# Performance work log

Hardware: AMD Instinct MI355X
Metric: run time of the kernel (lower is better)

## Reference

```python
import jax, jax.numpy as jnp
import numpy as np

D_MODEL = 512
PROJ = 2 * D_MODEL  # 1024
N_STATES = 32
KSIZE = 4
LN_EPS = 1e-3  # keras LayerNormalization default epsilon


def setup_inputs() -> dict:
    key = jax.random.key(0)
    ks = jax.random.split(key, 16)
    B, L = 2, 2048
    s_in = 1.0 / np.sqrt(D_MODEL)
    s_pr = 1.0 / np.sqrt(PROJ)
    x = jax.random.normal(ks[0], (B, L, D_MODEL), dtype=jnp.float32)
    # LayerNorm params
    ln_gamma = jnp.ones((D_MODEL,), jnp.float32)
    ln_beta = jnp.zeros((D_MODEL,), jnp.float32)
    # dense1 / dense2: d_model -> proj
    W1 = jax.random.normal(ks[1], (D_MODEL, PROJ), jnp.float32) * s_in
    b1 = jnp.zeros((PROJ,), jnp.float32)
    W2 = jax.random.normal(ks[2], (D_MODEL, PROJ), jnp.float32) * s_in
    b2 = jnp.zeros((PROJ,), jnp.float32)
    # depthwise causal conv1d: kernel (K, 1, PROJ) in WIO layout, groups=PROJ
    conv_k = jax.random.normal(ks[3], (KSIZE, 1, PROJ), jnp.float32) * 0.5
    conv_b = jnp.zeros((PROJ,), jnp.float32)
    # SSM params
    A_log = jnp.log(jnp.broadcast_to(jnp.arange(1, N_STATES + 1, dtype=jnp.float32), (PROJ, N_STATES)))
    D_skip = jnp.ones((PROJ,), jnp.float32)
    WB = jax.random.normal(ks[4], (PROJ, N_STATES), jnp.float32) * s_pr
    bB = jnp.zeros((N_STATES,), jnp.float32)
    WC = jax.random.normal(ks[5], (PROJ, N_STATES), jnp.float32) * s_pr
    bC = jnp.zeros((N_STATES,), jnp.float32)
    Wd = jax.random.normal(ks[6], (PROJ, PROJ), jnp.float32) * s_pr
    bd = jnp.zeros((PROJ,), jnp.float32)
    # dense3: proj -> d_model
    W3 = jax.random.normal(ks[7], (PROJ, D_MODEL), jnp.float32) * s_pr
    b3 = jnp.zeros((D_MODEL,), jnp.float32)
    return dict(x=x, ln_gamma=ln_gamma, ln_beta=ln_beta, W1=W1, b1=b1, W2=W2, b2=b2,
                conv_k=conv_k, conv_b=conv_b, A_log=A_log, D_skip=D_skip,
                WB=WB, bB=bB, WC=WC, bC=bC, Wd=Wd, bd=bd, W3=W3, b3=b3)


def _layernorm(x, gamma, beta):
    mu = jnp.mean(x, axis=-1, keepdims=True)
    var = jnp.mean(jnp.square(x - mu), axis=-1, keepdims=True)
    return (x - mu) * jax.lax.rsqrt(var + LN_EPS) * gamma + beta


def _causal_dwconv(x, k, b):
    # x: [B,L,C], k: [K,1,C], depthwise causal conv (left-pad K-1)
    y = jax.lax.conv_general_dilated(
        x, k, window_strides=(1,), padding=[(KSIZE - 1, 0)],
        dimension_numbers=('NWC', 'WIO', 'NWC'), feature_group_count=PROJ)
    return y + b


def _selective_scan(u, delta, A, Bm, Cm, D_skip):
    # u, delta: [B,L,D]; A: [D,N]; Bm, Cm: [B,L,N]; D_skip: [D]
    deltaA = jnp.einsum('bld,dn->bldn', delta, A)                 # [B,L,D,N]
    deltaBu = jnp.einsum('bld,bld,bln->bldn', delta, u, Bm)        # [B,L,D,N]
    # shift deltaA left by one along L, zero at the end (pad trick in source)
    shifted = jnp.concatenate([deltaA[:, 1:], jnp.zeros_like(deltaA[:, :1])], axis=1)
    # reversed cumsum along L, then exp
    e = jnp.exp(jnp.flip(jnp.cumsum(jnp.flip(shifted, axis=1), axis=1), axis=1))
    xs = jnp.cumsum(deltaBu * e, axis=1) / (e + 1e-12)
    y = jnp.einsum('bldn,bln->bld', xs, Cm)
    return y + u * D_skip


def reference(x, ln_gamma, ln_beta, W1, b1, W2, b2, conv_k, conv_b,
              A_log, D_skip, WB, bB, WC, bC, Wd, bd, W3, b3):
    h = _layernorm(x, ln_gamma, ln_beta)
    x1 = h @ W1 + b1                      # [B,L,PROJ]
    x1 = _causal_dwconv(x1, conv_k, conv_b)
    x1 = jax.nn.silu(x1)
    A = -jnp.exp(A_log)                    # [PROJ,N]
    Cm = x1 @ WC + bC                      # [B,L,N]
    Bm = x1 @ WB + bB                      # [B,L,N]
    delta = jax.nn.softplus(x1 @ Wd + bd)  # [B,L,PROJ]
    y = _selective_scan(x1, delta, A, Bm, Cm, D_skip)
    x2 = jax.nn.silu(h @ W2 + b2)
    out = (y * x2) @ W3 + b3 + x           # residual; dropout is identity at inference
    return out
```

## Files before the change

### kernel.cpp

```cpp
#include <hip/hip_runtime.h>
#include <stdint.h>

#define L_SEQ 2048
#define BATCH 2
#define DMODEL 512
#define PROJ 1024
#define NST 32
#define NCAT 1152
#define ROWS (BATCH*L_SEQ)
#define THRESH 50.0f

typedef float f32x4 __attribute__((ext_vector_type(4)));
typedef short short8 __attribute__((ext_vector_type(8)));

__device__ inline float bf2f(unsigned short u){ uint32_t x=((uint32_t)u)<<16; float f; __builtin_memcpy(&f,&x,4); return f; }
__device__ inline unsigned short f2bf(float f){ uint32_t x; __builtin_memcpy(&x,&f,4); uint32_t r=x+0x7FFFu+((x>>16)&1u); return (unsigned short)(r>>16); }
__device__ inline float siluf(float x){ return x/(1.f+__expf(-x)); }
__device__ inline float softplusf(float x){ return x>20.f? x : log1pf(__expf(x)); }

#define AS1(p) ((const __attribute__((address_space(1))) void*)(p))
#define AS3(p) ((__attribute__((address_space(3))) void*)(p))

template<int N> __device__ inline void wait_vmcnt(){
  if constexpr (N==0)      asm volatile("s_waitcnt vmcnt(0)" ::: "memory");
  else if constexpr (N==1) asm volatile("s_waitcnt vmcnt(1)" ::: "memory");
  else if constexpr (N==2) asm volatile("s_waitcnt vmcnt(2)" ::: "memory");
  else if constexpr (N==3) asm volatile("s_waitcnt vmcnt(3)" ::: "memory");
  else if constexpr (N==4) asm volatile("s_waitcnt vmcnt(4)" ::: "memory");
  else if constexpr (N==5) asm volatile("s_waitcnt vmcnt(5)" ::: "memory");
  else if constexpr (N==6) asm volatile("s_waitcnt vmcnt(6)" ::: "memory");
  else                     asm volatile("s_waitcnt vmcnt(8)" ::: "memory");
}

__global__ __launch_bounds__(256)
void prep_kernel(const float* __restrict__ W1, const float* __restrict__ b1,
                 const float* __restrict__ W2, const float* __restrict__ b2,
                 const float* __restrict__ Wd, const float* __restrict__ bd,
                 const float* __restrict__ WB, const float* __restrict__ bB,
                 const float* __restrict__ WC, const float* __restrict__ bC,
                 const float* __restrict__ W3,
                 unsigned short* __restrict__ W12t, unsigned short* __restrict__ Wcatt,
                 unsigned short* __restrict__ W3t, float* __restrict__ bias12,
                 float* __restrict__ biascat)
{
  int i = blockIdx.x*256 + threadIdx.x;
  const int nA = 2048*512;
  const int nB = NCAT*1024;
  const int nC = 512*1024;
  if (i < nA) {
    int n = i >> 9, k = i & 511;
    float v = (n < 1024) ? W1[k*1024 + n] : W2[k*1024 + (n-1024)];
    W12t[i] = f2bf(v);
    return;
  }
  i -= nA;
  if (i < nB) {
    int n = i >> 10, k = i & 1023;
    float v;
    if (n < 1024) v = Wd[k*1024 + n];
    else if (n < 1056) v = WB[k*32 + (n-1024)];
    else if (n < 1088) v = WC[k*32 + (n-1056)];
    else v = 0.f;
    Wcatt[i] = f2bf(v);
    return;
  }
  i -= nB;
  if (i < nC) {
    int n = i >> 10, k = i & 1023;
    W3t[i] = f2bf(W3[k*512 + n]);
    return;
  }
  i -= nC;
  if (i < 2048) { bias12[i] = (i < 1024) ? b1[i] : b2[i-1024]; return; }
  i -= 2048;
  if (i < NCAT) {
    biascat[i] = (i < 1024) ? bd[i] : (i < 1056) ? bB[i-1024] : (i < 1088) ? bC[i-1056] : 0.f;
  }
}

__global__ __launch_bounds__(256)
void ln_kernel(const float* __restrict__ x, const float* __restrict__ gamma,
               const float* __restrict__ beta, unsigned short* __restrict__ H)
{
  int row = blockIdx.x*4 + (threadIdx.x >> 6);
  int lane = threadIdx.x & 63;
  const float4* xr = (const float4*)(x + (size_t)row*DMODEL);
  float4 v0 = xr[lane];
  float4 v1 = xr[lane+64];
  float s = v0.x+v0.y+v0.z+v0.w + v1.x+v1.y+v1.z+v1.w;
  float q = v0.x*v0.x+v0.y*v0.y+v0.z*v0.z+v0.w*v0.w
          + v1.x*v1.x+v1.y*v1.y+v1.z*v1.z+v1.w*v1.w;
#pragma unroll
  for (int m=32;m>0;m>>=1){ s += __shfl_xor(s,m); q += __shfl_xor(q,m); }
  float mu = s*(1.f/DMODEL);
  float var = q*(1.f/DMODEL) - mu*mu;
  float rs = rsqrtf(var + 1e-3f);
  int c0 = lane*4, c1 = 256 + lane*4;
  float4 g0 = *(const float4*)&gamma[c0]; float4 g1 = *(const float4*)&gamma[c1];
  float4 t0 = *(const float4*)&beta[c0];  float4 t1 = *(const float4*)&beta[c1];
  ushort4 o0, o1;
  o0.x = f2bf((v0.x-mu)*rs*g0.x + t0.x);
  o0.y = f2bf((v0.y-mu)*rs*g0.y + t0.y);
  o0.z = f2bf((v0.z-mu)*rs*g0.z + t0.z);
  o0.w = f2bf((v0.w-mu)*rs*g0.w + t0.w);
  o1.x = f2bf((v1.x-mu)*rs*g1.x + t1.x);
  o1.y = f2bf((v1.y-mu)*rs*g1.y + t1.y);
  o1.z = f2bf((v1.z-mu)*rs*g1.z + t1.z);
  o1.w = f2bf((v1.w-mu)*rs*g1.w + t1.w);
  *(ushort4*)&H[(size_t)row*DMODEL + c0] = o0;
  *(ushort4*)&H[(size_t)row*DMODEL + c1] = o1;
}

template<int BM, int BN, int WR, int WC, int MODE>
__global__ __launch_bounds__(256)
void gemm_bt(const unsigned short* __restrict__ A, const unsigned short* __restrict__ Bt,
             void* __restrict__ Cv, const float* __restrict__ bias,
             const float* __restrict__ res, int M, int N, int K)
{
  constexpr int BMW = BM/WR, BNW = BN/WC;
  constexpr int AM = BMW/16, AN = BNW/16;
  constexpr int ASEGI = BM*4/256;
  constexpr int BSEGI = BN*4/256;
  constexpr int LPT = ASEGI + BSEGI;
  __shared__ unsigned short As[3][BM*32];
  __shared__ unsigned short Bs[3][BN*32];
  int tid = threadIdx.x;
  int lane = tid & 63, wid = tid >> 6;
  int wm = wid / WC, wn = wid % WC;
  int m0 = blockIdx.x*BM, n0 = blockIdx.y*BN;

  f32x4 acc[AM][AN];
#pragma unroll
  for (int i=0;i<AM;i++)
#pragma unroll
    for (int j=0;j<AN;j++)
#pragma unroll
      for (int e=0;e<4;e++) acc[i][j][e] = 0.f;

  const unsigned short* ap[ASEGI];
  const unsigned short* bp[BSEGI];
#pragma unroll
  for (int j=0;j<ASEGI;j++){
    int s = tid + j*256;
    int row = s >> 2, kc = ((s & 3) ^ (row & 3)) * 8;
    ap[j] = A + (size_t)(m0+row)*K + kc;
  }
#pragma unroll
  for (int j=0;j<BSEGI;j++){
    int s = tid + j*256;
    int row = s >> 2, kc = ((s & 3) ^ (row & 3)) * 8;
    bp[j] = Bt + (size_t)(n0+row)*K + kc;
  }

  auto stage = [&](int buf){
#pragma unroll
    for (int j=0;j<ASEGI;j++){
      __builtin_amdgcn_global_load_lds(AS1(ap[j]), AS3(&As[buf][(size_t)(wid*64 + j*256)*8]), 16, 0, 0);
      ap[j] += 32;
    }
#pragma unroll
    for (int j=0;j<BSEGI;j++){
      __builtin_amdgcn_global_load_lds(AS1(bp[j]), AS3(&Bs[buf][(size_t)(wid*64 + j*256)*8]), 16, 0, 0);
      bp[j] += 32;
    }
  };

  stage(0);
  stage(1);
  int T = K/32;
  int rb = 0, wb = 2;
  int r = lane & 15, kb = lane >> 4;
  int kbx = kb ^ (r & 3);
  for (int t = 0; t < T; ++t) {
    if (t+1 < T) wait_vmcnt<LPT>();
    else         wait_vmcnt<0>();
    __builtin_amdgcn_s_barrier();
    if (t+2 < T) { stage(wb); wb = (wb==2)?0:wb+1; }
    short8 af[AM], bfr[AN];
#pragma unroll
    for (int i=0;i<AM;i++) af[i]  = *(const short8*)&As[rb][((wm*BMW + i*16 + r)*4 + kbx)*8];
#pragma unroll
    for (int j=0;j<AN;j++) bfr[j] = *(const short8*)&Bs[rb][((wn*BNW + j*16 + r)*4 + kbx)*8];
#pragma unroll
    for (int i=0;i<AM;i++)
#pragma unroll
      for (int j=0;j<AN;j++)
        acc[i][j] = __builtin_amdgcn_mfma_f32_16x16x32_bf16(af[i], bfr[j], acc[i][j], 0,0,0);
    rb = (rb==2)?0:rb+1;
  }

  int rr = (lane >> 4)*4, cc = lane & 15;
#pragma unroll
  for (int i=0;i<AM;i++)
#pragma unroll
    for (int j=0;j<AN;j++) {
      int col = n0 + wn*BNW + j*16 + cc;
      float bv = bias[col];
#pragma unroll
      for (int e=0;e<4;e++) {
        int row = m0 + wm*BMW + i*16 + rr + e;
        float v = acc[i][j][e] + bv;
        if (MODE == 0) {
          ((unsigned short*)Cv)[(size_t)row*N + col] = f2bf(v);
        } else if (MODE == 2) {
          if (col < 1024) v = softplusf(v);
          ((float*)Cv)[(size_t)row*N + col] = v;
        } else {
          v += res[(size_t)row*N + col];
          ((float*)Cv)[(size_t)row*N + col] = v;
        }
      }
    }
}

__global__ __launch_bounds__(256)
void conv_silu_kernel(const unsigned short* __restrict__ P12, const float* __restrict__ ck,
                      const float* __restrict__ cb, unsigned short* __restrict__ ubf,
                      unsigned short* __restrict__ x2bf)
{
  int gid = blockIdx.x*256 + threadIdx.x;
  int c4 = gid & 511;
  int row = gid >> 9;
  int l = row & (L_SEQ-1);
  if (c4 < 256) {
    int c = c4*4;
    float4 bv = *(const float4*)&cb[c];
    float r0=bv.x, r1=bv.y, r2=bv.z, r3=bv.w;
#pragma unroll
    for (int t=0;t<4;t++){
      int lsrc = l - 3 + t;
      if (lsrc >= 0) {
        ushort4 xv = *(const ushort4*)&P12[(size_t)(row-3+t)*2048 + c];
        float4 kv = *(const float4*)&ck[t*PROJ + c];
        r0 = fmaf(bf2f(xv.x),kv.x,r0);
        r1 = fmaf(bf2f(xv.y),kv.y,r1);
        r2 = fmaf(bf2f(xv.z),kv.z,r2);
        r3 = fmaf(bf2f(xv.w),kv.w,r3);
      }
    }
    ushort4 o;
    o.x=f2bf(siluf(r0)); o.y=f2bf(siluf(r1)); o.z=f2bf(siluf(r2)); o.w=f2bf(siluf(r3));
    *(ushort4*)&ubf[(size_t)row*PROJ + c] = o;
  } else {
    int c = (c4-256)*4;
    ushort4 xv = *(const ushort4*)&P12[(size_t)row*2048 + 1024 + c];
    ushort4 o;
    o.x=f2bf(siluf(bf2f(xv.x))); o.y=f2bf(siluf(bf2f(xv.y)));
    o.z=f2bf(siluf(bf2f(xv.z))); o.w=f2bf(siluf(bf2f(xv.w)));
    *(ushort4*)&x2bf[(size_t)row*PROJ + c] = o;
  }
}

__global__ __launch_bounds__(256)
void dtrans_kernel(const float* __restrict__ P3, float* __restrict__ deltaT)
{
  __shared__ float tile[32][33];
  int bz = blockIdx.z;
  int l0t = blockIdx.x*32, d0t = blockIdx.y*32;
  int lx = threadIdx.x & 31, ly = threadIdx.x >> 5;
#pragma unroll
  for (int i=0;i<4;i++)
    tile[ly+i*8][lx] = P3[(size_t)(bz*L_SEQ + l0t + ly + i*8)*NCAT + d0t + lx];
  __syncthreads();
#pragma unroll
  for (int i=0;i<4;i++)
    deltaT[(size_t)(bz*PROJ + d0t + ly + i*8)*L_SEQ + l0t + lx] = tile[lx][ly+i*8];
}

__global__ __launch_bounds__(256)
void tsum_kernel(const float* __restrict__ deltaT, float* __restrict__ sufshT,
                 int* __restrict__ l0out)
{
  int G = blockIdx.x;
  const float* row = deltaT + (size_t)G*L_SEQ;
  int t = threadIdx.x;
  float4 v0 = *(const float4*)&row[t*8];
  float4 v1 = *(const float4*)&row[t*8+4];
  float vals[8] = {v0.x,v0.y,v0.z,v0.w,v1.x,v1.y,v1.z,v1.w};
  float part = 0.f;
#pragma unroll
  for (int i=0;i<8;i++) part += vals[i];
  __shared__ float ps[256];
  ps[t] = part; __syncthreads();
  for (int off=1; off<256; off<<=1){
    float v = (t >= off) ? ps[t-off] : 0.f;
    __syncthreads();
    ps[t] += v;
    __syncthreads();
  }
  float T = ps[255];
  float prefx = ps[t] - part;
  float run = prefx; int cnt = 0; float out[8];
#pragma unroll
  for (int i=0;i<8;i++){
    float suf_l = T - run;
    cnt += (suf_l >= THRESH) ? 1 : 0;
    run += vals[i];
    out[i] = T - run;
  }
  *(float4*)&sufshT[(size_t)G*L_SEQ + t*8]     = make_float4(out[0],out[1],out[2],out[3]);
  *(float4*)&sufshT[(size_t)G*L_SEQ + t*8 + 4] = make_float4(out[4],out[5],out[6],out[7]);
  __shared__ int cs[256];
  cs[t] = cnt; __syncthreads();
  for (int off=128; off>0; off>>=1){ if (t < off) cs[t] += cs[t+off]; __syncthreads(); }
  if (t == 0) {
    int total = cs[0];
    l0out[G] = total > 0 ? total-1 : 0;
  }
}

__global__ __launch_bounds__(256)
void scan_kernel(const float* __restrict__ deltaT, const float* __restrict__ sufshT,
                 const float* __restrict__ P3, const unsigned short* __restrict__ ubf,
                 const float* __restrict__ A_log, const int* __restrict__ l0arr,
                 float* __restrict__ ystate)
{
  int tid = threadIdx.x;
  int n = tid & 31;
  int G = blockIdx.x*8 + (tid >> 5);
  int b = G >> 10, d = G & 1023;
  float np1 = __expf(A_log[d*NST + n]);
  int myl0 = l0arr[G];
  int base = min(myl0, __shfl_xor(myl0, 32)) & ~7;
  const float* dT = deltaT + (size_t)G*L_SEQ;
  const float* sT = sufshT + (size_t)G*L_SEQ;
  const float* P3b = P3 + (size_t)b*L_SEQ*NCAT + 1024 + n;
  const unsigned short* ub = ubf + (size_t)b*L_SEQ*PROJ + d;
  float* yb = ystate + (size_t)b*L_SEQ*PROJ + d;
  float s = 0.f;
  for (int l = base; l < L_SEQ; l += 8) {
    float4 d0 = *(const float4*)&dT[l];
    float4 d1 = *(const float4*)&dT[l+4];
    float4 f0 = *(const float4*)&sT[l];
    float4 f1 = *(const float4*)&sT[l+4];
    float dl[8] = {d0.x,d0.y,d0.z,d0.w,d1.x,d1.y,d1.z,d1.w};
    float sf[8] = {f0.x,f0.y,f0.z,f0.w,f1.x,f1.y,f1.z,f1.w};
    float uu[8], Bv[8], Cv[8];
#pragma unroll
    for (int t=0;t<8;t++){
      uu[t] = bf2f(ub[(size_t)(l+t)*PROJ]);
      const float* rp = P3b + (size_t)(l+t)*NCAT;
      Bv[t] = rp[0];
      Cv[t] = rp[32];
    }
#pragma unroll
    for (int t=0;t<8;t++){
      float decay = __expf(-dl[t]*np1);
      s = fmaf(decay, s, dl[t]*uu[t]*Bv[t]);
      float gte = 1.f/(1.f + 1e-12f*__expf(np1*sf[t]));
      float contrib = s*gte*Cv[t];
#pragma unroll
      for (int m=16;m>0;m>>=1) contrib += __shfl_xor(contrib, m);
      if (n == 0) yb[(size_t)(l+t)*PROJ] = contrib;
    }
  }
}

__global__ __launch_bounds__(256)
void zmul_kernel(const float* __restrict__ ystate, const unsigned short* __restrict__ ubf,
                 const unsigned short* __restrict__ x2bf, const float* __restrict__ Dskip,
                 unsigned short* __restrict__ zbf)
{
  size_t i = ((size_t)blockIdx.x*256 + threadIdx.x)*4;
  int d = (int)(i & (PROJ-1));
  float4 ys = *(const float4*)&ystate[i];
  ushort4 uu = *(const ushort4*)&ubf[i];
  ushort4 xx = *(const ushort4*)&x2bf[i];
  float4 Dv = *(const float4*)&Dskip[d];
  ushort4 o;
  o.x = f2bf((ys.x + bf2f(uu.x)*Dv.x)*bf2f(xx.x));
  o.y = f2bf((ys.y + bf2f(uu.y)*Dv.y)*bf2f(xx.y));
  o.z = f2bf((ys.z + bf2f(uu.z)*Dv.z)*bf2f(xx.z));
  o.w = f2bf((ys.w + bf2f(uu.w)*Dv.w)*bf2f(xx.w));
  *(ushort4*)&zbf[i] = o;
}

extern "C" void kernel_launch(void* const* d_in, const int* in_sizes, int n_in,
                              void* d_out, int out_size, void* d_ws, size_t ws_size,
                              hipStream_t stream)
{
  const float* x     = (const float*)d_in[0];
  const float* ln_g  = (const float*)d_in[1];
  const float* ln_b  = (const float*)d_in[2];
  const float* W1    = (const float*)d_in[3];
  const float* b1    = (const float*)d_in[4];
  const float* W2    = (const float*)d_in[5];
  const float* b2    = (const float*)d_in[6];
  const float* convk = (const float*)d_in[7];
  const float* convb = (const float*)d_in[8];
  const float* A_log = (const float*)d_in[9];
  const float* Dskip = (const float*)d_in[10];
  const float* WB    = (const float*)d_in[11];
  const float* bB    = (const float*)d_in[12];
  const float* WC    = (const float*)d_in[13];
  const float* bC    = (const float*)d_in[14];
  const float* Wd    = (const float*)d_in[15];
  const float* bd    = (const float*)d_in[16];
  const float* W3    = (const float*)d_in[17];
  const float* b3    = (const float*)d_in[18];

  char* w = (char*)d_ws;
  auto alloc = [&](size_t bytes){ char* p = w; w += (bytes + 255) & ~(size_t)255; return p; };
  unsigned short* Hbf    = (unsigned short*)alloc((size_t)ROWS*DMODEL*2);
  unsigned short* W12t   = (unsigned short*)alloc((size_t)2048*512*2);
  unsigned short* Wcatt  = (unsigned short*)alloc((size_t)NCAT*1024*2);
  unsigned short* W3t    = (unsigned short*)alloc((size_t)512*1024*2);
  float*          bias12 = (float*)alloc(2048*4);
  float*          biascat= (float*)alloc(NCAT*4);
  unsigned short* P12    = (unsigned short*)alloc((size_t)ROWS*2048*2);
  unsigned short* ubf    = (unsigned short*)alloc((size_t)ROWS*PROJ*2);
  unsigned short* x2bf   = (unsigned short*)alloc((size_t)ROWS*PROJ*2);
  float*          P3     = (float*)alloc((size_t)ROWS*NCAT*4);
  float*          deltaT = (float*)alloc((size_t)2048*L_SEQ*4);
  float*          sufshT = (float*)alloc((size_t)2048*L_SEQ*4);
  int*            l0arr  = (int*)alloc(2048*4);
  float*          ystate = (float*)alloc((size_t)ROWS*PROJ*4);
  unsigned short* zbf    = (unsigned short*)alloc((size_t)ROWS*PROJ*2);

  {
    int total = 2048*512 + NCAT*1024 + 512*1024 + 2048 + NCAT;
    prep_kernel<<<(total+255)/256, 256, 0, stream>>>(W1,b1,W2,b2,Wd,bd,WB,bB,WC,bC,W3,
                                                     W12t,Wcatt,W3t,bias12,biascat);
  }
  ln_kernel<<<ROWS/4, 256, 0, stream>>>(x, ln_g, ln_b, Hbf);

  dim3 g1(ROWS/64, 2048/128);
  gemm_bt<64,128,2,2,0><<<g1, 256, 0, stream>>>(Hbf, W12t, P12, bias12, nullptr, ROWS, 2048, DMODEL);

  conv_silu_kernel<<<ROWS*512/256, 256, 0, stream>>>(P12, convk, convb, ubf, x2bf);

  dim3 g2(ROWS/64, NCAT/64);
  gemm_bt<64,64,2,2,2><<<g2, 256, 0, stream>>>(ubf, Wcatt, P3, biascat, nullptr, ROWS, NCAT, PROJ);

  hipMemsetAsync(ystate, 0, (size_t)ROWS*PROJ*4, stream);

  dim3 gt(L_SEQ/32, PROJ/32, BATCH);
  dtrans_kernel<<<gt, 256, 0, stream>>>(P3, deltaT);

  tsum_kernel<<<2048, 256, 0, stream>>>(deltaT, sufshT, l0arr);

  scan_kernel<<<2048/8, 256, 0, stream>>>(deltaT, sufshT, P3, ubf, A_log, l0arr, ystate);

  zmul_kernel<<<(ROWS*PROJ/4)/256, 256, 0, stream>>>(ystate, ubf, x2bf, Dskip, zbf);

  dim3 g3(ROWS/64, DMODEL/64);
  gemm_bt<64,64,2,2,3><<<g3, 256, 0, stream>>>(zbf, W3t, (float*)d_out, b3, x, ROWS, DMODEL, PROJ);
}
```

Baseline: 163.6 us.

## Retile GEMMs to 2-wave row-split blocks and drop ystate memset via l0 masking

The GEMM kernel is restructured so each block uses a configurable number of waves, each owning a stripe of rows across the full block width. The first two GEMMs move to 128x64 tiles with 128 threads, and the last to 64x64 with 128 threads. Separately, the memset that zeroed the scan output buffer is removed; the elementwise z kernel now masks ystate entries before each channel's l0 start index, avoiding a full-buffer write. Smaller blocks change occupancy and per-wave register use, and correctness now depends on the scan not leaving stale data beyond the masked region.

```diff
diff --git a/kernel.cpp b/kernel.cpp
--- a/kernel.cpp
+++ b/kernel.cpp
@@ -111,22 +111,22 @@
   *(ushort4*)&H[(size_t)row*DMODEL + c1] = o1;
 }
 
-template<int BM, int BN, int WR, int WC, int MODE>
-__global__ __launch_bounds__(256)
+template<int BM, int BN, int WAVES, int MODE>
+__global__ __launch_bounds__(WAVES*64)
 void gemm_bt(const unsigned short* __restrict__ A, const unsigned short* __restrict__ Bt,
              void* __restrict__ Cv, const float* __restrict__ bias,
              const float* __restrict__ res, int M, int N, int K)
 {
-  constexpr int BMW = BM/WR, BNW = BN/WC;
-  constexpr int AM = BMW/16, AN = BNW/16;
-  constexpr int ASEGI = BM*4/256;
-  constexpr int BSEGI = BN*4/256;
+  constexpr int THREADS = WAVES*64;
+  constexpr int BMW = BM/WAVES;
+  constexpr int AM = BMW/16, AN = BN/16;
+  constexpr int ASEGI = BM*4/THREADS;
+  constexpr int BSEGI = BN*4/THREADS;
   constexpr int LPT = ASEGI + BSEGI;
   __shared__ unsigned short As[3][BM*32];
   __shared__ unsigned short Bs[3][BN*32];
   int tid = threadIdx.x;
   int lane = tid & 63, wid = tid >> 6;
-  int wm = wid / WC, wn = wid % WC;
   int m0 = blockIdx.x*BM, n0 = blockIdx.y*BN;
 
   f32x4 acc[AM][AN];
@@ -141,13 +141,13 @@
   const unsigned short* bp[BSEGI];
 #pragma unroll
   for (int j=0;j<ASEGI;j++){
-    int s = tid + j*256;
+    int s = tid + j*THREADS;
     int row = s >> 2, kc = ((s & 3) ^ (row & 3)) * 8;
     ap[j] = A + (size_t)(m0+row)*K + kc;
   }
 #pragma unroll
   for (int j=0;j<BSEGI;j++){
-    int s = tid + j*256;
+    int s = tid + j*THREADS;
     int row = s >> 2, kc = ((s & 3) ^ (row & 3)) * 8;
     bp[j] = Bt + (size_t)(n0+row)*K + kc;
   }
@@ -155,12 +155,12 @@
   auto stage = [&](int buf){
 #pragma unroll
     for (int j=0;j<ASEGI;j++){
-      __builtin_amdgcn_global_load_lds(AS1(ap[j]), AS3(&As[buf][(size_t)(wid*64 + j*256)*8]), 16, 0, 0);
+      __builtin_amdgcn_global_load_lds(AS1(ap[j]), AS3(&As[buf][(size_t)(j*THREADS + wid*64)*8]), 16, 0, 0);
       ap[j] += 32;
     }
 #pragma unroll
     for (int j=0;j<BSEGI;j++){
-      __builtin_amdgcn_global_load_lds(AS1(bp[j]), AS3(&Bs[buf][(size_t)(wid*64 + j*256)*8]), 16, 0, 0);
+      __builtin_amdgcn_global_load_lds(AS1(bp[j]), AS3(&Bs[buf][(size_t)(j*THREADS + wid*64)*8]), 16, 0, 0);
       bp[j] += 32;
     }
   };
@@ -178,9 +178,9 @@
     if (t+2 < T) { stage(wb); wb = (wb==2)?0:wb+1; }
     short8 af[AM], bfr[AN];
 #pragma unroll
-    for (int i=0;i<AM;i++) af[i]  = *(const short8*)&As[rb][((wm*BMW + i*16 + r)*4 + kbx)*8];
-#pragma unroll
-    for (int j=0;j<AN;j++) bfr[j] = *(const short8*)&Bs[rb][((wn*BNW + j*16 + r)*4 + kbx)*8];
+    for (int i=0;i<AM;i++) af[i]  = *(const short8*)&As[rb][((wid*BMW + i*16 + r)*4 + kbx)*8];
+#pragma unroll
+    for (int j=0;j<AN;j++) bfr[j] = *(const short8*)&Bs[rb][((j*16 + r)*4 + kbx)*8];
 #pragma unroll
     for (int i=0;i<AM;i++)
 #pragma unroll
@@ -194,11 +194,11 @@
   for (int i=0;i<AM;i++)
 #pragma unroll
     for (int j=0;j<AN;j++) {
-      int col = n0 + wn*BNW + j*16 + cc;
+      int col = n0 + j*16 + cc;
       float bv = bias[col];
 #pragma unroll
       for (int e=0;e<4;e++) {
-        int row = m0 + wm*BMW + i*16 + rr + e;
+        int row = m0 + wid*BMW + i*16 + rr + e;
         float v = acc[i][j][e] + bv;
         if (MODE == 0) {
           ((unsigned short*)Cv)[(size_t)row*N + col] = f2bf(v);
@@ -359,11 +359,19 @@
 __global__ __launch_bounds__(256)
 void zmul_kernel(const float* __restrict__ ystate, const unsigned short* __restrict__ ubf,
                  const unsigned short* __restrict__ x2bf, const float* __restrict__ Dskip,
-                 unsigned short* __restrict__ zbf)
+                 const int* __restrict__ l0arr, unsigned short* __restrict__ zbf)
 {
   size_t i = ((size_t)blockIdx.x*256 + threadIdx.x)*4;
   int d = (int)(i & (PROJ-1));
+  int row = (int)(i >> 10);
+  int l = row & (L_SEQ-1);
+  int b = row >> 11;
+  int4 l0v = *(const int4*)&l0arr[b*PROJ + d];
   float4 ys = *(const float4*)&ystate[i];
+  ys.x = (l >= l0v.x) ? ys.x : 0.f;
+  ys.y = (l >= l0v.y) ? ys.y : 0.f;
+  ys.z = (l >= l0v.z) ? ys.z : 0.f;
+  ys.w = (l >= l0v.w) ? ys.w : 0.f;
   ushort4 uu = *(const ushort4*)&ubf[i];
   ushort4 xx = *(const ushort4*)&x2bf[i];
   float4 Dv = *(const float4*)&Dskip[d];
@@ -424,15 +432,13 @@
   }
   ln_kernel<<<ROWS/4, 256, 0, stream>>>(x, ln_g, ln_b, Hbf);
 
-  dim3 g1(ROWS/64, 2048/128);
-  gemm_bt<64,128,2,2,0><<<g1, 256, 0, stream>>>(Hbf, W12t, P12, bias12, nullptr, ROWS, 2048, DMODEL);
+  dim3 g1(ROWS/128, 2048/64);
+  gemm_bt<128,64,2,0><<<g1, 128, 0, stream>>>(Hbf, W12t, P12, bias12, nullptr, ROWS, 2048, DMODEL);
 
   conv_silu_kernel<<<ROWS*512/256, 256, 0, stream>>>(P12, convk, convb, ubf, x2bf);
 
-  dim3 g2(ROWS/64, NCAT/64);
-  gemm_bt<64,64,2,2,2><<<g2, 256, 0, stream>>>(ubf, Wcatt, P3, biascat, nullptr, ROWS, NCAT, PROJ);
-
-  hipMemsetAsync(ystate, 0, (size_t)ROWS*PROJ*4, stream);
+  dim3 g2(ROWS/128, NCAT/64);
+  gemm_bt<128,64,2,2><<<g2, 128, 0, stream>>>(ubf, Wcatt, P3, biascat, nullptr, ROWS, NCAT, PROJ);
 
   dim3 gt(L_SEQ/32, PROJ/32, BATCH);
   dtrans_kernel<<<gt, 256, 0, stream>>>(P3, deltaT);
@@ -441,8 +447,8 @@
 
   scan_kernel<<<2048/8, 256, 0, stream>>>(deltaT, sufshT, P3, ubf, A_log, l0arr, ystate);
 
-  zmul_kernel<<<(ROWS*PROJ/4)/256, 256, 0, stream>>>(ystate, ubf, x2bf, Dskip, zbf);
+  zmul_kernel<<<(ROWS*PROJ/4)/256, 256, 0, stream>>>(ystate, ubf, x2bf, Dskip, l0arr, zbf);
 
   dim3 g3(ROWS/64, DMODEL/64);
-  gemm_bt<64,64,2,2,3><<<g3, 256, 0, stream>>>(zbf, W3t, (float*)d_out, b3, x, ROWS, DMODEL, PROJ);
-}
+  gemm_bt<64,64,2,3><<<g3, 128, 0, stream>>>(zbf, W3t, (float*)d_out, b3, x, ROWS, DMODEL, PROJ);
+}
```

New measurement: 179.5 us. 9.7% more time.

## Compute delta/B/C GEMM transposed, drop transpose kernel and per-step suffix buffer

Applied to the files above, without the earlier changes.

The second GEMM now swaps its operands so it writes delta, B and C directly in a channel-major (transposed) layout. This removes the separate transpose kernel and the strided per-timestep B/C loads in the scan. The suffix-sum buffer is shrunk to one value per 8-step chunk, and the scan rebuilds per-step values from a running cumulative sum. The ystate memset is replaced by masking rows below l0 in zmul, and the first GEMM's tile size is changed. The risks are slightly different floating-point rounding in the rebuilt suffix sums and a new dependence on the l0 masking being correct.

```diff
diff --git a/kernel.cpp b/kernel.cpp
--- a/kernel.cpp
+++ b/kernel.cpp
@@ -155,12 +155,12 @@
   auto stage = [&](int buf){
 #pragma unroll
     for (int j=0;j<ASEGI;j++){
-      __builtin_amdgcn_global_load_lds(AS1(ap[j]), AS3(&As[buf][(size_t)(wid*64 + j*256)*8]), 16, 0, 0);
+      __builtin_amdgcn_global_load_lds(AS1(ap[j]), AS3(&As[buf][(size_t)(j*256 + wid*64)*8]), 16, 0, 0);
       ap[j] += 32;
     }
 #pragma unroll
     for (int j=0;j<BSEGI;j++){
-      __builtin_amdgcn_global_load_lds(AS1(bp[j]), AS3(&Bs[buf][(size_t)(wid*64 + j*256)*8]), 16, 0, 0);
+      __builtin_amdgcn_global_load_lds(AS1(bp[j]), AS3(&Bs[buf][(size_t)(j*256 + wid*64)*8]), 16, 0, 0);
       bp[j] += 32;
     }
   };
@@ -195,18 +195,23 @@
 #pragma unroll
     for (int j=0;j<AN;j++) {
       int col = n0 + wn*BNW + j*16 + cc;
-      float bv = bias[col];
+      float bcol = (MODE == 4) ? 0.f : bias[col];
 #pragma unroll
       for (int e=0;e<4;e++) {
         int row = m0 + wm*BMW + i*16 + rr + e;
-        float v = acc[i][j][e] + bv;
-        if (MODE == 0) {
-          ((unsigned short*)Cv)[(size_t)row*N + col] = f2bf(v);
-        } else if (MODE == 2) {
+        float v = acc[i][j][e];
+        if constexpr (MODE == 4) {
+          v += bias[row];
+          if (row < 1024) v = softplusf(v);
+          ((float*)Cv)[(size_t)row*N + col] = v;
+        } else if constexpr (MODE == 0) {
+          ((unsigned short*)Cv)[(size_t)row*N + col] = f2bf(v + bcol);
+        } else if constexpr (MODE == 2) {
+          v += bcol;
           if (col < 1024) v = softplusf(v);
           ((float*)Cv)[(size_t)row*N + col] = v;
         } else {
-          v += res[(size_t)row*N + col];
+          v += bcol + res[(size_t)row*N + col];
           ((float*)Cv)[(size_t)row*N + col] = v;
         }
       }
@@ -252,27 +257,12 @@
 }
 
 __global__ __launch_bounds__(256)
-void dtrans_kernel(const float* __restrict__ P3, float* __restrict__ deltaT)
-{
-  __shared__ float tile[32][33];
-  int bz = blockIdx.z;
-  int l0t = blockIdx.x*32, d0t = blockIdx.y*32;
-  int lx = threadIdx.x & 31, ly = threadIdx.x >> 5;
-#pragma unroll
-  for (int i=0;i<4;i++)
-    tile[ly+i*8][lx] = P3[(size_t)(bz*L_SEQ + l0t + ly + i*8)*NCAT + d0t + lx];
-  __syncthreads();
-#pragma unroll
-  for (int i=0;i<4;i++)
-    deltaT[(size_t)(bz*PROJ + d0t + ly + i*8)*L_SEQ + l0t + lx] = tile[lx][ly+i*8];
-}
-
-__global__ __launch_bounds__(256)
-void tsum_kernel(const float* __restrict__ deltaT, float* __restrict__ sufshT,
+void tsum_kernel(const float* __restrict__ CT, float* __restrict__ suf8,
                  int* __restrict__ l0out)
 {
   int G = blockIdx.x;
-  const float* row = deltaT + (size_t)G*L_SEQ;
+  int b = G >> 10, d = G & 1023;
+  const float* row = CT + (size_t)d*ROWS + b*L_SEQ;
   int t = threadIdx.x;
   float4 v0 = *(const float4*)&row[t*8];
   float4 v1 = *(const float4*)&row[t*8+4];
@@ -290,16 +280,14 @@
   }
   float T = ps[255];
   float prefx = ps[t] - part;
-  float run = prefx; int cnt = 0; float out[8];
+  suf8[(size_t)G*(L_SEQ/8) + t] = T - prefx;
+  float run = prefx; int cnt = 0;
 #pragma unroll
   for (int i=0;i<8;i++){
     float suf_l = T - run;
     cnt += (suf_l >= THRESH) ? 1 : 0;
     run += vals[i];
-    out[i] = T - run;
-  }
-  *(float4*)&sufshT[(size_t)G*L_SEQ + t*8]     = make_float4(out[0],out[1],out[2],out[3]);
-  *(float4*)&sufshT[(size_t)G*L_SEQ + t*8 + 4] = make_float4(out[4],out[5],out[6],out[7]);
+  }
   __shared__ int cs[256];
   cs[t] = cnt; __syncthreads();
   for (int off=128; off>0; off>>=1){ if (t < off) cs[t] += cs[t+off]; __syncthreads(); }
@@ -310,10 +298,9 @@
 }
 
 __global__ __launch_bounds__(256)
-void scan_kernel(const float* __restrict__ deltaT, const float* __restrict__ sufshT,
-                 const float* __restrict__ P3, const unsigned short* __restrict__ ubf,
-                 const float* __restrict__ A_log, const int* __restrict__ l0arr,
-                 float* __restrict__ ystate)
+void scan_kernel(const float* __restrict__ CT, const float* __restrict__ suf8,
+                 const unsigned short* __restrict__ ubf, const float* __restrict__ A_log,
+                 const int* __restrict__ l0arr, float* __restrict__ ystate)
 {
   int tid = threadIdx.x;
   int n = tid & 31;
@@ -322,32 +309,34 @@
   float np1 = __expf(A_log[d*NST + n]);
   int myl0 = l0arr[G];
   int base = min(myl0, __shfl_xor(myl0, 32)) & ~7;
-  const float* dT = deltaT + (size_t)G*L_SEQ;
-  const float* sT = sufshT + (size_t)G*L_SEQ;
-  const float* P3b = P3 + (size_t)b*L_SEQ*NCAT + 1024 + n;
+  const float* dT = CT + (size_t)d*ROWS + b*L_SEQ;
+  const float* Br = CT + (size_t)(1024+n)*ROWS + b*L_SEQ;
+  const float* Cr = CT + (size_t)(1056+n)*ROWS + b*L_SEQ;
+  const float* s8 = suf8 + (size_t)G*(L_SEQ/8);
   const unsigned short* ub = ubf + (size_t)b*L_SEQ*PROJ + d;
   float* yb = ystate + (size_t)b*L_SEQ*PROJ + d;
   float s = 0.f;
   for (int l = base; l < L_SEQ; l += 8) {
     float4 d0 = *(const float4*)&dT[l];
     float4 d1 = *(const float4*)&dT[l+4];
-    float4 f0 = *(const float4*)&sT[l];
-    float4 f1 = *(const float4*)&sT[l+4];
+    float4 B0 = *(const float4*)&Br[l];
+    float4 B1 = *(const float4*)&Br[l+4];
+    float4 C0 = *(const float4*)&Cr[l];
+    float4 C1 = *(const float4*)&Cr[l+4];
+    float sufv = s8[l >> 3];
     float dl[8] = {d0.x,d0.y,d0.z,d0.w,d1.x,d1.y,d1.z,d1.w};
-    float sf[8] = {f0.x,f0.y,f0.z,f0.w,f1.x,f1.y,f1.z,f1.w};
-    float uu[8], Bv[8], Cv[8];
+    float Bv[8] = {B0.x,B0.y,B0.z,B0.w,B1.x,B1.y,B1.z,B1.w};
+    float Cv[8] = {C0.x,C0.y,C0.z,C0.w,C1.x,C1.y,C1.z,C1.w};
+    float uu[8];
+#pragma unroll
+    for (int t=0;t<8;t++) uu[t] = bf2f(ub[(size_t)(l+t)*PROJ]);
+    float cum = 0.f;
 #pragma unroll
     for (int t=0;t<8;t++){
-      uu[t] = bf2f(ub[(size_t)(l+t)*PROJ]);
-      const float* rp = P3b + (size_t)(l+t)*NCAT;
-      Bv[t] = rp[0];
-      Cv[t] = rp[32];
-    }
-#pragma unroll
-    for (int t=0;t<8;t++){
+      cum += dl[t];
       float decay = __expf(-dl[t]*np1);
       s = fmaf(decay, s, dl[t]*uu[t]*Bv[t]);
-      float gte = 1.f/(1.f + 1e-12f*__expf(np1*sf[t]));
+      float gte = 1.f/(1.f + 1e-12f*__expf(np1*(sufv - cum)));
       float contrib = s*gte*Cv[t];
 #pragma unroll
       for (int m=16;m>0;m>>=1) contrib += __shfl_xor(contrib, m);
@@ -359,11 +348,19 @@
 __global__ __launch_bounds__(256)
 void zmul_kernel(const float* __restrict__ ystate, const unsigned short* __restrict__ ubf,
                  const unsigned short* __restrict__ x2bf, const float* __restrict__ Dskip,
-                 unsigned short* __restrict__ zbf)
+                 const int* __restrict__ l0arr, unsigned short* __restrict__ zbf)
 {
   size_t i = ((size_t)blockIdx.x*256 + threadIdx.x)*4;
   int d = (int)(i & (PROJ-1));
+  int row = (int)(i >> 10);
+  int l = row & (L_SEQ-1);
+  int b = row >> 11;
+  int4 l0v = *(const int4*)&l0arr[b*PROJ + d];
   float4 ys = *(const float4*)&ystate[i];
+  ys.x = (l >= l0v.x) ? ys.x : 0.f;
+  ys.y = (l >= l0v.y) ? ys.y : 0.f;
+  ys.z = (l >= l0v.z) ? ys.z : 0.f;
+  ys.w = (l >= l0v.w) ? ys.w : 0.f;
   ushort4 uu = *(const ushort4*)&ubf[i];
   ushort4 xx = *(const ushort4*)&x2bf[i];
   float4 Dv = *(const float4*)&Dskip[d];
@@ -410,9 +407,8 @@
   unsigned short* P12    = (unsigned short*)alloc((size_t)ROWS*2048*2);
   unsigned short* ubf    = (unsigned short*)alloc((size_t)ROWS*PROJ*2);
   unsigned short* x2bf   = (unsigned short*)alloc((size_t)ROWS*PROJ*2);
-  float*          P3     = (float*)alloc((size_t)ROWS*NCAT*4);
-  float*          deltaT = (float*)alloc((size_t)2048*L_SEQ*4);
-  float*          sufshT = (float*)alloc((size_t)2048*L_SEQ*4);
+  float*          CT     = (float*)alloc((size_t)NCAT*ROWS*4);
+  float*          suf8   = (float*)alloc((size_t)2048*(L_SEQ/8)*4);
   int*            l0arr  = (int*)alloc(2048*4);
   float*          ystate = (float*)alloc((size_t)ROWS*PROJ*4);
   unsigned short* zbf    = (unsigned short*)alloc((size_t)ROWS*PROJ*2);
@@ -424,24 +420,19 @@
   }
   ln_kernel<<<ROWS/4, 256, 0, stream>>>(x, ln_g, ln_b, Hbf);
 
-  dim3 g1(ROWS/64, 2048/128);
-  gemm_bt<64,128,2,2,0><<<g1, 256, 0, stream>>>(Hbf, W12t, P12, bias12, nullptr, ROWS, 2048, DMODEL);
+  dim3 g1(ROWS/64, 2048/64);
+  gemm_bt<64,64,2,2,0><<<g1, 256, 0, stream>>>(Hbf, W12t, P12, bias12, nullptr, ROWS, 2048, DMODEL);
 
   conv_silu_kernel<<<ROWS*512/256, 256, 0, stream>>>(P12, convk, convb, ubf, x2bf);
 
-  dim3 g2(ROWS/64, NCAT/64);
-  gemm_bt<64,64,2,2,2><<<g2, 256, 0, stream>>>(ubf, Wcatt, P3, biascat, nullptr, ROWS, NCAT, PROJ);
-
-  hipMemsetAsync(ystate, 0, (size_t)ROWS*PROJ*4, stream);
-
-  dim3 gt(L_SEQ/32, PROJ/32, BATCH);
-  dtrans_kernel<<<gt, 256, 0, stream>>>(P3, deltaT);
-
-  tsum_kernel<<<2048, 256, 0, stream>>>(deltaT, sufshT, l0arr);
-
-  scan_kernel<<<2048/8, 256, 0, stream>>>(deltaT, sufshT, P3, ubf, A_log, l0arr, ystate);
-
-  zmul_kernel<<<(ROWS*PROJ/4)/256, 256, 0, stream>>>(ystate, ubf, x2bf, Dskip, zbf);
+  dim3 g2(NCAT/64, ROWS/64);
+  gemm_bt<64,64,2,2,4><<<g2, 256, 0, stream>>>(Wcatt, ubf, CT, biascat, nullptr, NCAT, ROWS, PROJ);
+
+  tsum_kernel<<<2048, 256, 0, stream>>>(CT, suf8, l0arr);
+
+  scan_kernel<<<2048/8, 256, 0, stream>>>(CT, suf8, ubf, A_log, l0arr, ystate);
+
+  zmul_kernel<<<(ROWS*PROJ/4)/256, 256, 0, stream>>>(ystate, ubf, x2bf, Dskip, l0arr, zbf);
 
   dim3 g3(ROWS/64, DMODEL/64);
   gemm_bt<64,64,2,2,3><<<g3, 256, 0, stream>>>(zbf, W3t, (float*)d_out, b3, x, ROWS, DMODEL, PROJ);
```

After: 162.6 us. Within noise of the previous version (-0.6%).
